# Kernel optimization log

Measured on AMD Instinct MI355X. Metric: run time of the kernel, lower is better.

## Reference

```python
import jax, jax.numpy as jnp
import numpy as np

N = 100000       # nodes
E = 1600000      # edges
NFEAT, NHID, NCLASS = 512, 256, 40
NLAYERS = 10     # APPNP propagation steps K
ALPHA = 0.1      # teleport probability


def setup_inputs() -> dict:
    key = jax.random.key(0)
    ks = jax.random.split(key, 8)
    x = jax.random.normal(ks[0], (N, NFEAT), jnp.float32)
    row = jax.random.randint(ks[1], (E,), 0, N, jnp.int32)
    col = jax.random.randint(ks[2], (E,), 0, N, jnp.int32)
    vals = jax.random.uniform(ks[3], (E,), jnp.float32)
    # MyLinear init: uniform(-stdv, stdv) with stdv = 1/sqrt(in_features);
    # bias is a shape-[1] scalar (faithful to torch.FloatTensor([out_features])).
    s1 = 1.0 / np.sqrt(NFEAT)
    s2 = 1.0 / np.sqrt(NHID)
    W1 = jax.random.uniform(ks[4], (NFEAT, NHID), jnp.float32, -s1, s1)
    b1 = jax.random.uniform(ks[5], (1,), jnp.float32, -s1, s1)
    W2 = jax.random.uniform(ks[6], (NHID, NCLASS), jnp.float32, -s2, s2)
    b2 = jax.random.uniform(ks[7], (1,), jnp.float32, -s2, s2)
    return dict(x=x, row=row, col=col, vals=vals, W1=W1, b1=b1, W2=W2, b2=b2)


def reference(x, row, col, vals, W1, b1, W2, b2):
    # 2-layer MLP (eval mode: dropout inactive, no BN)
    h = jax.nn.relu(x @ W1 + b1)          # [N, NHID]
    h = h @ W2 + b2                        # [N, NCLASS]

    # sparse adjacency spmm via edge-list segment sum
    def spmm(z):
        return jax.ops.segment_sum(vals[:, None] * z[col], row, num_segments=N)

    # APPNP propagation: z <- (1-alpha) * A z + alpha * h
    def step(z, _):
        z = (1.0 - ALPHA) * spmm(z) + ALPHA * h
        return z, None

    z, _ = jax.lax.scan(step, h, None, length=NLAYERS)
    return jax.nn.log_softmax(z, axis=1)
```

## Files before the change

### kernel.cpp

```cpp
#include <hip/hip_runtime.h>


typedef unsigned short ushort_t;
typedef short short8 __attribute__((ext_vector_type(8)));
typedef float f32x4 __attribute__((ext_vector_type(4)));

#define NFEAT 512
#define NHID 256
#define NCLASS 40

static __device__ __forceinline__ float b2f(ushort_t u) {
    unsigned v = ((unsigned)u) << 16;
    float f;
    __builtin_memcpy(&f, &v, 4);
    return f;
}
static __device__ __forceinline__ ushort_t f2b(float f) {
    unsigned u;
    __builtin_memcpy(&u, &f, 4);
    unsigned r = u + 0x7FFFu + ((u >> 16) & 1u);
    return (ushort_t)(r >> 16);
}
static __device__ __forceinline__ ushort_t san_u(ushort_t u) {
    return ((u & 0x7F80u) == 0x7F80u) ? (ushort_t)0 : u;
}
static __device__ __forceinline__ float ldmix(const void* p, size_t i, int isbf) {
    if (isbf) return b2f(san_u(((const ushort_t*)p)[i]));
    return ((const float*)p)[i];
}
static __device__ __forceinline__ float ldz(const void* p, size_t i, int zbf) {
    return zbf ? b2f(((const ushort_t*)p)[i]) : ((const float*)p)[i];
}
static __device__ __forceinline__ void stz(void* p, size_t i, int zbf, float v) {
    if (zbf) ((ushort_t*)p)[i] = f2b(v);
    else ((float*)p)[i] = v;
}

__global__ void detect_kernel(const ushort_t* __restrict__ x, int* __restrict__ flag) {
    __shared__ int cnt_s;
    if (threadIdx.x == 0) cnt_s = 0;
    __syncthreads();
    int c = 0;
    for (int i = threadIdx.x; i < 2048; i += 256) {
        ushort_t u = x[2 * i];
        int e = (u >> 7) & 0xFF;
        if (e >= 107 && e <= 141) c++;
    }
    atomicAdd(&cnt_s, c);
    __syncthreads();
    if (threadIdx.x == 0) flag[0] = (cnt_s >= 1024) ? 1 : 0;
}


__global__ void zero_kernel(int* __restrict__ p, int n) {
    int i = blockIdx.x * 256 + threadIdx.x;
    if (i < n) p[i] = 0;
}

__global__ void hist_kernel(const int* __restrict__ row, int* __restrict__ deg, int e, int n) {
    int i = blockIdx.x * 256 + threadIdx.x;
    if (i < e) {
        int r = row[i];
        if ((unsigned)r < (unsigned)n) atomicAdd(&deg[r], 1);
    }
}

__global__ void scan_blocksum(const int* __restrict__ deg, int* __restrict__ bsum, int n) {
    __shared__ int s[256];
    int t = threadIdx.x;
    int i = blockIdx.x * 256 + t;
    s[t] = (i < n) ? deg[i] : 0;
    __syncthreads();
    for (int o = 128; o; o >>= 1) {
        if (t < o) s[t] += s[t + o];
        __syncthreads();
    }
    if (t == 0) bsum[blockIdx.x] = s[0];
}

__global__ void scan_bsum_excl(int* __restrict__ bsum, int nb) {
    __shared__ int s[512];
    int t = threadIdx.x;
    int v = (t < nb) ? bsum[t] : 0;
    int own = v;
    s[t] = v;
    __syncthreads();
    for (int o = 1; o < 512; o <<= 1) {
        int add = (t >= o) ? s[t - o] : 0;
        __syncthreads();
        s[t] += add;
        __syncthreads();
    }
    if (t < nb) bsum[t] = s[t] - own;
}

__global__ void scan_emit(const int* __restrict__ deg, const int* __restrict__ bsum,
                          int* __restrict__ row_start, int* __restrict__ cursor, int n) {
    __shared__ int s[256];
    int t = threadIdx.x;
    int i = blockIdx.x * 256 + t;
    int v = (i < n) ? deg[i] : 0;
    int own = v;
    s[t] = v;
    __syncthreads();
    for (int o = 1; o < 256; o <<= 1) {
        int add = (t >= o) ? s[t - o] : 0;
        __syncthreads();
        s[t] += add;
        __syncthreads();
    }
    if (i < n) {
        int rs = bsum[blockIdx.x] + s[t] - own;
        row_start[i] = rs;
        cursor[i] = rs;
    }
}

__global__ void scatter_kernel(const int* __restrict__ row, const int* __restrict__ col,
                               const void* __restrict__ vals, int* __restrict__ cursor,
                               int* __restrict__ cs_col, void* __restrict__ cs_val,
                               const int* __restrict__ flag, int zbf, int e, int n) {
    int i = blockIdx.x * 256 + threadIdx.x;
    if (i < e) {
        int isbf = flag[0];
        int r = row[i];
        if ((unsigned)r >= (unsigned)n) return;
        int p = atomicAdd(&cursor[r], 1);
        if ((unsigned)p < (unsigned)e) {
            int c = col[i];
            cs_col[p] = ((unsigned)c < (unsigned)n) ? c : 0;
            stz(cs_val, p, zbf, ldmix(vals, i, isbf));
        }
    }
}


__global__ void w1frag_kernel(const void* __restrict__ W1, ushort_t* __restrict__ w1f,
                              const int* __restrict__ flag) {
    int t = blockIdx.x * 256 + threadIdx.x;
    if (t >= 16 * 16 * 64) return;
    int isbf = flag[0];
    int l = t & 63, nt = (t >> 6) & 15, kb = t >> 10;
    ushort_t tmp[8];
#pragma unroll
    for (int j = 0; j < 8; j++) {
        int k = kb * 32 + (l >> 4) * 8 + j;
        int nn = nt * 16 + (l & 15);
        tmp[j] = f2b(ldmix(W1, (size_t)k * NHID + nn, isbf));
    }
    *(short8*)(w1f + (size_t)t * 8) = *(short8*)tmp;
}

__global__ void w2frag_kernel(const void* __restrict__ W2, ushort_t* __restrict__ w2f,
                              const int* __restrict__ flag) {
    int t = blockIdx.x * 256 + threadIdx.x;
    if (t >= 8 * 3 * 64) return;
    int isbf = flag[0];
    int l = t % 64;
    int nt = (t / 64) % 3;
    int kb = t / 192;
    ushort_t tmp[8];
#pragma unroll
    for (int j = 0; j < 8; j++) {
        int k = kb * 32 + (l >> 4) * 8 + j;
        int nn = nt * 16 + (l & 15);
        tmp[j] = (nn < NCLASS) ? f2b(ldmix(W2, (size_t)k * NCLASS + nn, isbf)) : (ushort_t)0;
    }
    *(short8*)(w2f + (size_t)t * 8) = *(short8*)tmp;
}


__global__ __launch_bounds__(256) void mlp_kernel(const void* __restrict__ x,
                                                  const ushort_t* __restrict__ w1f,
                                                  const ushort_t* __restrict__ w2f,
                                                  const void* __restrict__ b1,
                                                  const void* __restrict__ b2,
                                                  void* __restrict__ h,
                                                  const int* __restrict__ flag, int zbf, int n) {
    __shared__ ushort_t Alds[64][40];
    __shared__ ushort_t Hlds[64][264];
    const int t = threadIdx.x;
    const int isbf = flag[0];
    const int wv = t >> 6, l = t & 63;
    const int lq = l >> 4, lr = l & 15;
    const int m0 = blockIdx.x * 64;

    f32x4 acc[16];
#pragma unroll
    for (int i = 0; i < 16; i++) acc[i] = (f32x4){0.f, 0.f, 0.f, 0.f};

    const int rS = t >> 2, qS = t & 3;
    int rowS = m0 + rS;
    if (rowS > n - 1) rowS = n - 1;
    const size_t xbase = (size_t)rowS * NFEAT + qS * 8;
    const ushort_t* aldsp = &Alds[wv * 16 + lr][lq * 8];

    for (int kb = 0; kb < 16; kb++) {
        short8 av;
        if (isbf) {
            av = *(const short8*)((const ushort_t*)x + xbase + kb * 32);
#pragma unroll
            for (int j = 0; j < 8; j++) {
                ushort_t u = (ushort_t)av[j];
                if ((u & 0x7F80u) == 0x7F80u) av[j] = 0;
            }
        } else {
            const float* xf = (const float*)x + xbase + kb * 32;
            f32x4 a0 = *(const f32x4*)xf;
            f32x4 a1 = *(const f32x4*)(xf + 4);
#pragma unroll
            for (int j = 0; j < 4; j++) {
                av[j] = (short)f2b(a0[j]);
                av[4 + j] = (short)f2b(a1[j]);
            }
        }
        *(short8*)&Alds[rS][qS * 8] = av;
        __syncthreads();
        short8 afrag = *(const short8*)aldsp;
        const ushort_t* bp = w1f + ((size_t)(kb * 16) * 64 + l) * 8;
#pragma unroll
        for (int nt = 0; nt < 16; nt++) {
            short8 bfrag = *(const short8*)(bp + (size_t)nt * 64 * 8);
            acc[nt] = __builtin_amdgcn_mfma_f32_16x16x32_bf16(afrag, bfrag, acc[nt], 0, 0, 0);
        }
        __syncthreads();
    }

    float bias1 = ldmix(b1, 0, isbf);
#pragma unroll
    for (int nt = 0; nt < 16; nt++) {
#pragma unroll
        for (int i = 0; i < 4; i++) {
            float v = acc[nt][i] + bias1;
            v = fmaxf(v, 0.f);
            Hlds[wv * 16 + lq * 4 + i][nt * 16 + lr] = f2b(v);
        }
    }
    __syncthreads();

    f32x4 acc2[3];
#pragma unroll
    for (int i = 0; i < 3; i++) acc2[i] = (f32x4){0.f, 0.f, 0.f, 0.f};
    const ushort_t* hp = &Hlds[wv * 16 + lr][lq * 8];
#pragma unroll
    for (int kb = 0; kb < 8; kb++) {
        short8 afrag = *(const short8*)(hp + kb * 32);
#pragma unroll
        for (int nt = 0; nt < 3; nt++) {
            short8 bfrag = *(const short8*)(w2f + ((size_t)(kb * 3 + nt) * 64 + l) * 8);
            acc2[nt] = __builtin_amdgcn_mfma_f32_16x16x32_bf16(afrag, bfrag, acc2[nt], 0, 0, 0);
        }
    }

    float bias2 = ldmix(b2, 0, isbf);
#pragma unroll
    for (int nt = 0; nt < 3; nt++) {
#pragma unroll
        for (int i = 0; i < 4; i++) {
            int rowg = m0 + wv * 16 + lq * 4 + i;
            int colg = nt * 16 + lr;
            if (rowg < n && colg < NCLASS)
                stz(h, (size_t)rowg * NCLASS + colg, zbf, acc2[nt][i] + bias2);
        }
    }
}


template <int ZBF>
__global__ __launch_bounds__(256) void prop_kernel(const void* __restrict__ zin,
                                                   void* __restrict__ zout,
                                                   const void* __restrict__ h,
                                                   const int* __restrict__ row_start,
                                                   const int* __restrict__ deg,
                                                   const int* __restrict__ cs_col,
                                                   const void* __restrict__ cs_val, int n) {
    int w = blockIdx.x * 4 + (threadIdx.x >> 6);
    int lane = threadIdx.x & 63;
    if (w >= n) return;
    int start = row_start[w];
    int d = deg[w];
    const bool laneok = lane < NCLASS;
    float acc = 0.f;
    for (int base = 0; base < d; base += 64) {
        int m = d - base;
        if (m > 64) m = 64;
        int c = 0;
        float v = 0.f;
        if (lane < m) {
            size_t idx = (size_t)start + base + lane;
            c = cs_col[idx];
            v = ZBF ? b2f(((const ushort_t*)cs_val)[idx]) : ((const float*)cs_val)[idx];
        }
        for (int j = 0; j < m; j += 8) {
            int cc[8];
            float vv[8];
#pragma unroll
            for (int k = 0; k < 8; k++) {
                cc[k] = __shfl(c, j + k);
                vv[k] = __shfl(v, j + k);
            }
            if (laneok) {
                float zv[8];
#pragma unroll
                for (int k = 0; k < 8; k++) {
                    size_t zi = (size_t)cc[k] * NCLASS + lane;
                    zv[k] = ZBF ? b2f(((const ushort_t*)zin)[zi]) : ((const float*)zin)[zi];
                }
#pragma unroll
                for (int k = 0; k < 8; k++) acc += vv[k] * zv[k];
            }
        }
    }
    if (laneok) {
        float hv = ZBF ? b2f(((const ushort_t*)h)[(size_t)w * NCLASS + lane])
                       : ((const float*)h)[(size_t)w * NCLASS + lane];
        float r = 0.9f * acc + 0.1f * hv;
        if (ZBF) ((ushort_t*)zout)[(size_t)w * NCLASS + lane] = f2b(r);
        else ((float*)zout)[(size_t)w * NCLASS + lane] = r;
    }
}


__global__ __launch_bounds__(256) void lsm_kernel(const void* __restrict__ z,
                                                  void* __restrict__ out,
                                                  const int* __restrict__ flag, int zbf, int n) {
    int w = blockIdx.x * 4 + (threadIdx.x >> 6);
    int lane = threadIdx.x & 63;
    if (w >= n) return;
    int isbf = flag[0];
    float v = (lane < NCLASS) ? ldz(z, (size_t)w * NCLASS + lane, zbf) : -INFINITY;
    float m = v;
    for (int o = 32; o; o >>= 1) m = fmaxf(m, __shfl_xor(m, o));
    float e = (lane < NCLASS) ? __expf(v - m) : 0.f;
    float s = e;
    for (int o = 32; o; o >>= 1) s += __shfl_xor(s, o);
    if (lane < NCLASS) {
        float r = v - m - __logf(s);
        if (isbf) ((ushort_t*)out)[(size_t)w * NCLASS + lane] = f2b(r);
        else ((float*)out)[(size_t)w * NCLASS + lane] = r;
    }
}


extern "C" void kernel_launch(void* const* d_in, const int* in_sizes, int n_in, void* d_out,
                              int out_size, void* d_ws, size_t ws_size, hipStream_t stream) {
    const void* x = d_in[0];
    const int* row = (const int*)d_in[1];
    const int* col = (const int*)d_in[2];
    const void* vals = d_in[3];
    const void* W1 = d_in[4];
    const void* b1 = d_in[5];
    const void* W2 = d_in[6];
    const void* b2 = d_in[7];

    const int N = in_sizes[0] / NFEAT;
    const int E = in_sizes[1];

    const int roomy = (ws_size == 0) || (ws_size >= (size_t)66 * 1024 * 1024);
    const int zbf = roomy ? 0 : 1;
    const size_t ez = roomy ? 4 : 2;

    char* ws = (char*)d_ws;
    size_t off = 0;
    auto take = [&](size_t bytes) {
        size_t o = off;
        off = (off + bytes + 255) & ~(size_t)255;
        return (void*)(ws + o);
    };
    void* h = take((size_t)N * NCLASS * ez);
    void* zA = take((size_t)N * NCLASS * ez);
    void* zB = take((size_t)N * NCLASS * ez);
    int* cs_col = (int*)take((size_t)E * 4);
    void* cs_val = take((size_t)E * ez);
    int* deg = (int*)take((size_t)N * 4);
    int* row_start = (int*)take((size_t)N * 4);
    int* cursor = (int*)take((size_t)N * 4);
    ushort_t* w1f = (ushort_t*)take((size_t)NFEAT * NHID * 2);
    ushort_t* w2f = (ushort_t*)take((size_t)8 * 3 * 64 * 8 * 2);
    int* bsum = (int*)take(512 * 4);
    int* flag = (int*)take(256);

    const int NB = (N + 255) / 256;
    const int EB = (E + 255) / 256;
    const int GB = (N + 63) / 64;
    const int PB = (N + 3) / 4;

    detect_kernel<<<1, 256, 0, stream>>>((const ushort_t*)x, flag);

    zero_kernel<<<(N + 255) / 256, 256, 0, stream>>>(deg, N);
    hist_kernel<<<EB, 256, 0, stream>>>(row, deg, E, N);
    scan_blocksum<<<NB, 256, 0, stream>>>(deg, bsum, N);
    scan_bsum_excl<<<1, 512, 0, stream>>>(bsum, NB);
    scan_emit<<<NB, 256, 0, stream>>>(deg, bsum, row_start, cursor, N);
    scatter_kernel<<<EB, 256, 0, stream>>>(row, col, vals, cursor, cs_col, cs_val, flag, zbf, E,
                                           N);

    w1frag_kernel<<<64, 256, 0, stream>>>(W1, w1f, flag);
    w2frag_kernel<<<6, 256, 0, stream>>>(W2, w2f, flag);

    mlp_kernel<<<GB, 256, 0, stream>>>(x, w1f, w2f, b1, b2, h, flag, zbf, N);

    if (zbf) {
        prop_kernel<1><<<PB, 256, 0, stream>>>(h, zA, h, row_start, deg, cs_col, cs_val, N);
        const void* zi = zA;
        void* zo = zB;
        for (int s = 1; s < 10; s++) {
            prop_kernel<1><<<PB, 256, 0, stream>>>(zi, zo, h, row_start, deg, cs_col, cs_val, N);
            const void* tmp = zi;
            zi = zo;
            zo = (void*)tmp;
        }
        lsm_kernel<<<PB, 256, 0, stream>>>(zi, d_out, flag, zbf, N);
    } else {
        prop_kernel<0><<<PB, 256, 0, stream>>>(h, zA, h, row_start, deg, cs_col, cs_val, N);
        const void* zi = zA;
        void* zo = zB;
        for (int s = 1; s < 10; s++) {
            prop_kernel<0><<<PB, 256, 0, stream>>>(zi, zo, h, row_start, deg, cs_col, cs_val, N);
            const void* tmp = zi;
            zi = zo;
            zo = (void*)tmp;
        }
        lsm_kernel<<<PB, 256, 0, stream>>>(zi, d_out, flag, zbf, N);
    }
}
```

Measured before the change: 1.140 ms.

## Force bf16 propagation state, double-buffer MLP GEMM via LDS, widen SpMM gather

Always stores h, z and edge values in bf16, dropping the fp32 path that ran when workspace was large. This halves gather traffic in the ten propagation passes but adds rounding error to every step. The MLP GEMM now double-buffers x tiles and W1 fragments in LDS, fetching W1 with direct global-to-LDS loads to overlap fetch with MFMA, and sets a three-blocks-per-CU launch bound. The SpMM inner loop issues sixteen gathers per batch instead of eight, and the row index is made wave-uniform.

After: 1.059 ms. -7.1%, faster.

```diff
diff --git a/kernel.cpp b/kernel.cpp
--- a/kernel.cpp
+++ b/kernel.cpp
@@ -34,6 +34,12 @@
 static __device__ __forceinline__ void stz(void* p, size_t i, int zbf, float v) {
     if (zbf) ((ushort_t*)p)[i] = f2b(v);
     else ((float*)p)[i] = v;
+}
+
+static __device__ __forceinline__ void gld_lds16(const ushort_t* g, ushort_t* l) {
+    __builtin_amdgcn_global_load_lds(
+        (const __attribute__((address_space(1))) unsigned int*)g,
+        (__attribute__((address_space(3))) unsigned int*)l, 16, 0, 0);
 }
 
 __global__ void detect_kernel(const ushort_t* __restrict__ x, int* __restrict__ flag) {
@@ -170,61 +176,114 @@
 }
 
 
-__global__ __launch_bounds__(256) void mlp_kernel(const void* __restrict__ x,
-                                                  const ushort_t* __restrict__ w1f,
-                                                  const ushort_t* __restrict__ w2f,
-                                                  const void* __restrict__ b1,
-                                                  const void* __restrict__ b2,
-                                                  void* __restrict__ h,
-                                                  const int* __restrict__ flag, int zbf, int n) {
-    __shared__ ushort_t Alds[64][40];
-    __shared__ ushort_t Hlds[64][264];
+template <int ISBF>
+static __device__ __forceinline__ short8 load_afrag(const void* __restrict__ x, size_t base) {
+    short8 av;
+    if (ISBF) {
+        av = *(const short8*)((const ushort_t*)x + base);
+#pragma unroll
+        for (int j = 0; j < 8; j++) {
+            ushort_t u = (ushort_t)av[j];
+            if ((u & 0x7F80u) == 0x7F80u) av[j] = 0;
+        }
+    } else {
+        const float* xf = (const float*)x + base;
+        f32x4 a0 = *(const f32x4*)xf;
+        f32x4 a1 = *(const f32x4*)(xf + 4);
+#pragma unroll
+        for (int j = 0; j < 4; j++) {
+            av[j] = (short)f2b(a0[j]);
+            av[4 + j] = (short)f2b(a1[j]);
+        }
+    }
+    return av;
+}
+
+#define APITCH 42
+
+template <int ISBF>
+static __device__ __forceinline__ void gemm1_staged(const void* __restrict__ x,
+                                                    const ushort_t* __restrict__ w1f,
+                                                    size_t xbase, ushort_t* Bl0, ushort_t* Bl1,
+                                                    ushort_t* awr0, ushort_t* awr1,
+                                                    const ushort_t* ard0, const ushort_t* ard1,
+                                                    const ushort_t* brd0, const ushort_t* brd1,
+                                                    f32x4 (&acc)[16], int wv, int l) {
+    {
+        short8 a0 = load_afrag<ISBF>(x, xbase);
+        *(short8*)awr0 = a0;
+        const ushort_t* src = w1f + (size_t)wv * 512 + (size_t)l * 8;
+#pragma unroll
+        for (int i = 0; i < 4; i++) gld_lds16(src + i * 2048, Bl0 + wv * 512 + i * 2048);
+    }
+    __syncthreads();
+
+#pragma unroll
+    for (int kb = 0; kb < 16; kb++) {
+        const bool even = (kb & 1) == 0;
+        const ushort_t* brd = even ? brd0 : brd1;
+        const ushort_t* ard = even ? ard0 : ard1;
+        ushort_t* awrn = even ? awr1 : awr0;
+        ushort_t* bln = even ? Bl1 : Bl0;
+        short8 an;
+        if (kb < 15) {
+            an = load_afrag<ISBF>(x, xbase + (size_t)(kb + 1) * 32);
+            const ushort_t* src =
+                w1f + (size_t)(kb + 1) * 8192 + (size_t)wv * 512 + (size_t)l * 8;
+#pragma unroll
+            for (int i = 0; i < 4; i++) gld_lds16(src + i * 2048, bln + wv * 512 + i * 2048);
+        }
+        short8 af = *(const short8*)ard;
+#pragma unroll
+        for (int nt = 0; nt < 16; nt++) {
+            short8 bf = *(const short8*)(brd + nt * 512);
+            acc[nt] = __builtin_amdgcn_mfma_f32_16x16x32_bf16(af, bf, acc[nt], 0, 0, 0);
+        }
+        if (kb < 15) *(short8*)awrn = an;
+        __syncthreads();
+    }
+}
+
+__global__ __launch_bounds__(256, 3) void mlp_kernel(const void* __restrict__ x,
+                                                     const ushort_t* __restrict__ w1f,
+                                                     const ushort_t* __restrict__ w2f,
+                                                     const void* __restrict__ b1,
+                                                     const void* __restrict__ b2,
+                                                     void* __restrict__ h,
+                                                     const int* __restrict__ flag, int zbf,
+                                                     int n) {
+    __shared__ __align__(16) ushort_t pool[21760];
+    ushort_t* Bl0 = pool;
+    ushort_t* Bl1 = pool + 8192;
+    ushort_t* Al0 = pool + 16384;
+    ushort_t* Al1 = pool + 16384 + 2688;
+    ushort_t* Hl = pool;
+
     const int t = threadIdx.x;
     const int isbf = flag[0];
     const int wv = t >> 6, l = t & 63;
     const int lq = l >> 4, lr = l & 15;
     const int m0 = blockIdx.x * 64;
 
-    f32x4 acc[16];
-#pragma unroll
-    for (int i = 0; i < 16; i++) acc[i] = (f32x4){0.f, 0.f, 0.f, 0.f};
-
     const int rS = t >> 2, qS = t & 3;
     int rowS = m0 + rS;
     if (rowS > n - 1) rowS = n - 1;
-    const size_t xbase = (size_t)rowS * NFEAT + qS * 8;
-    const ushort_t* aldsp = &Alds[wv * 16 + lr][lq * 8];
-
-    for (int kb = 0; kb < 16; kb++) {
-        short8 av;
-        if (isbf) {
-            av = *(const short8*)((const ushort_t*)x + xbase + kb * 32);
-#pragma unroll
-            for (int j = 0; j < 8; j++) {
-                ushort_t u = (ushort_t)av[j];
-                if ((u & 0x7F80u) == 0x7F80u) av[j] = 0;
-            }
-        } else {
-            const float* xf = (const float*)x + xbase + kb * 32;
-            f32x4 a0 = *(const f32x4*)xf;
-            f32x4 a1 = *(const f32x4*)(xf + 4);
-#pragma unroll
-            for (int j = 0; j < 4; j++) {
-                av[j] = (short)f2b(a0[j]);
-                av[4 + j] = (short)f2b(a1[j]);
-            }
-        }
-        *(short8*)&Alds[rS][qS * 8] = av;
-        __syncthreads();
-        short8 afrag = *(const short8*)aldsp;
-        const ushort_t* bp = w1f + ((size_t)(kb * 16) * 64 + l) * 8;
-#pragma unroll
-        for (int nt = 0; nt < 16; nt++) {
-            short8 bfrag = *(const short8*)(bp + (size_t)nt * 64 * 8);
-            acc[nt] = __builtin_amdgcn_mfma_f32_16x16x32_bf16(afrag, bfrag, acc[nt], 0, 0, 0);
-        }
-        __syncthreads();
-    }
+    const size_t xbase = (size_t)rowS * NFEAT + (size_t)qS * 8;
+    ushort_t* awr0 = Al0 + rS * APITCH + qS * 8;
+    ushort_t* awr1 = Al1 + rS * APITCH + qS * 8;
+    const ushort_t* ard0 = Al0 + (wv * 16 + lr) * APITCH + lq * 8;
+    const ushort_t* ard1 = Al1 + (wv * 16 + lr) * APITCH + lq * 8;
+    const ushort_t* brd0 = Bl0 + l * 8;
+    const ushort_t* brd1 = Bl1 + l * 8;
+
+    f32x4 acc[16];
+#pragma unroll
+    for (int i = 0; i < 16; i++) acc[i] = (f32x4){0.f, 0.f, 0.f, 0.f};
+
+    if (isbf)
+        gemm1_staged<1>(x, w1f, xbase, Bl0, Bl1, awr0, awr1, ard0, ard1, brd0, brd1, acc, wv, l);
+    else
+        gemm1_staged<0>(x, w1f, xbase, Bl0, Bl1, awr0, awr1, ard0, ard1, brd0, brd1, acc, wv, l);
 
     float bias1 = ldmix(b1, 0, isbf);
 #pragma unroll
@@ -233,7 +292,7 @@
         for (int i = 0; i < 4; i++) {
             float v = acc[nt][i] + bias1;
             v = fmaxf(v, 0.f);
-            Hlds[wv * 16 + lq * 4 + i][nt * 16 + lr] = f2b(v);
+            Hl[(wv * 16 + lq * 4 + i) * 264 + nt * 16 + lr] = f2b(v);
         }
     }
     __syncthreads();
@@ -241,7 +300,7 @@
     f32x4 acc2[3];
 #pragma unroll
     for (int i = 0; i < 3; i++) acc2[i] = (f32x4){0.f, 0.f, 0.f, 0.f};
-    const ushort_t* hp = &Hlds[wv * 16 + lr][lq * 8];
+    const ushort_t* hp = Hl + (wv * 16 + lr) * 264 + lq * 8;
 #pragma unroll
     for (int kb = 0; kb < 8; kb++) {
         short8 afrag = *(const short8*)(hp + kb * 32);
@@ -277,8 +336,9 @@
     int w = blockIdx.x * 4 + (threadIdx.x >> 6);
     int lane = threadIdx.x & 63;
     if (w >= n) return;
-    int start = row_start[w];
-    int d = deg[w];
+    int wu = __builtin_amdgcn_readfirstlane(w);
+    int start = row_start[wu];
+    int d = deg[wu];
     const bool laneok = lane < NCLASS;
     float acc = 0.f;
     for (int base = 0; base < d; base += 64) {
@@ -291,23 +351,23 @@
             c = cs_col[idx];
             v = ZBF ? b2f(((const ushort_t*)cs_val)[idx]) : ((const float*)cs_val)[idx];
         }
-        for (int j = 0; j < m; j += 8) {
-            int cc[8];
-            float vv[8];
-#pragma unroll
-            for (int k = 0; k < 8; k++) {
+        for (int j = 0; j < m; j += 16) {
+            int cc[16];
+            float vv[16];
+#pragma unroll
+            for (int k = 0; k < 16; k++) {
                 cc[k] = __shfl(c, j + k);
                 vv[k] = __shfl(v, j + k);
             }
             if (laneok) {
-                float zv[8];
-#pragma unroll
-                for (int k = 0; k < 8; k++) {
+                float zv[16];
+#pragma unroll
+                for (int k = 0; k < 16; k++) {
                     size_t zi = (size_t)cc[k] * NCLASS + lane;
                     zv[k] = ZBF ? b2f(((const ushort_t*)zin)[zi]) : ((const float*)zin)[zi];
                 }
 #pragma unroll
-                for (int k = 0; k < 8; k++) acc += vv[k] * zv[k];
+                for (int k = 0; k < 16; k++) acc += vv[k] * zv[k];
             }
         }
     }
@@ -356,9 +416,8 @@
     const int N = in_sizes[0] / NFEAT;
     const int E = in_sizes[1];
 
-    const int roomy = (ws_size == 0) || (ws_size >= (size_t)66 * 1024 * 1024);
-    const int zbf = roomy ? 0 : 1;
-    const size_t ez = roomy ? 4 : 2;
+    const int zbf = 1;
+    const size_t ez = 2;
 
     char* ws = (char*)d_ws;
     size_t off = 0;
@@ -400,8 +459,8 @@
 
     mlp_kernel<<<GB, 256, 0, stream>>>(x, w1f, w2f, b1, b2, h, flag, zbf, N);
 
-    if (zbf) {
-        prop_kernel<1><<<PB, 256, 0, stream>>>(h, zA, h, row_start, deg, cs_col, cs_val, N);
+    prop_kernel<1><<<PB, 256, 0, stream>>>(h, zA, h, row_start, deg, cs_col, cs_val, N);
+    {
         const void* zi = zA;
         void* zo = zB;
         for (int s = 1; s < 10; s++) {
@@ -411,16 +470,5 @@
             zo = (void*)tmp;
         }
         lsm_kernel<<<PB, 256, 0, stream>>>(zi, d_out, flag, zbf, N);
-    } else {
-        prop_kernel<0><<<PB, 256, 0, stream>>>(h, zA, h, row_start, deg, cs_col, cs_val, N);
-        const void* zi = zA;
-        void* zo = zB;
-        for (int s = 1; s < 10; s++) {
-            prop_kernel<0><<<PB, 256, 0, stream>>>(zi, zo, h, row_start, deg, cs_col, cs_val, N);
-            const void* tmp = zi;
-            zi = zo;
-            zo = (void*)tmp;
-        }
-        lsm_kernel<<<PB, 256, 0, stream>>>(zi, d_out, flag, zbf, N);
-    }
-}
+    }
+}
```
